# Performance work log

Measured on AMD Instinct MI355X. Metric: run time of the kernel, lower is better.

The kernel has to match this reference:

```python
import jax, jax.numpy as jnp
import numpy as np

N, G, NPG, K = 65536, 64, 1024, 32
NB, BD, IN_CH, GNN_DIM, L = 64, 4, 256, 256, 2
NBP = (BD - 1) * BD // 2 * NB  # 384
E = 524288


def setup_inputs():
    key = jax.random.key(0)
    ks = jax.random.split(key, 10)
    s = 0.05
    return {
        "x": jax.random.normal(ks[0], (N, IN_CH), jnp.float32),
        "eigvec": jax.random.normal(ks[1], (N, K), jnp.float32) / np.float32(np.sqrt(NPG)),
        "eigval": jax.random.uniform(ks[2], (G, K), jnp.float32, 0.0, 2.0),
        "taus": jnp.ones((NB,), jnp.float32),
        "enc_w": jax.random.normal(ks[3], (IN_CH, GNN_DIM), jnp.float32) * s,
        "enc_b": jnp.zeros((GNN_DIM,), jnp.float32),
        "self_w": jax.random.normal(ks[4], (L, GNN_DIM, GNN_DIM), jnp.float32) * s,
        "self_b": jnp.zeros((L, GNN_DIM), jnp.float32),
        "nb_w": jax.random.normal(ks[5], (L, GNN_DIM, GNN_DIM), jnp.float32) * s,
        "nb_b": jnp.zeros((L, GNN_DIM), jnp.float32),
        "dec_w": jax.random.normal(ks[6], (GNN_DIM, NBP), jnp.float32) * s,
        "dec_b": jnp.zeros((NBP,), jnp.float32),
        "lin_w": jax.random.normal(ks[7], (IN_CH, IN_CH), jnp.float32) * s,
        "lin_b": jnp.zeros((IN_CH,), jnp.float32),
        "edge_index": jax.random.randint(ks[8], (2, E), 0, N, jnp.int32),
    }


def _householder(p):
    # p: [M, BD*(BD-1)//2] -> Q: [M, BD, BD], product of BD-1 Householder reflectors
    M = p.shape[0]
    Q = jnp.broadcast_to(jnp.eye(BD, dtype=p.dtype), (M, BD, BD))
    idx = 0
    for j in range(BD - 1):  # small fixed loop over bundle_dim-1 reflectors
        n = BD - 1 - j
        v = jnp.zeros((M, BD), p.dtype).at[:, j].set(1.0)
        v = v.at[:, j + 1:].set(p[:, idx:idx + n])
        idx += n
        nrm = jnp.sum(v * v, axis=1)[:, None, None]
        Qv = jnp.einsum('mij,mj->mi', Q, v)
        Q = Q - 2.0 * Qv[:, :, None] * v[:, None, :] / nrm
    return Q


def reference(x, eigvec, eigval, taus, enc_w, enc_b, self_w, self_b,
              nb_w, nb_b, dec_w, dec_b, lin_w, lin_b, edge_index):
    gelu = lambda t: jax.nn.gelu(t, approximate=False)
    src, dst = edge_index[0], edge_index[1]
    vf = x.reshape(N, NB, BD, -1)                      # [N, NB, BD, 1]
    # SumGNN structural encoder: h = gelu(enc(x)); residual GNN layers; dec
    h = gelu(x @ enc_w + enc_b)
    for k in range(L):
        agg = jax.ops.segment_sum(h[src], dst, num_segments=N)  # sum aggregation
        hk = (h @ self_w[k] + self_b[k]) + (agg @ nb_w[k] + nb_b[k])
        h = gelu(hk) + h
    node_rep = h @ dec_w + dec_b                       # [N, NBP]
    Q = _householder(node_rep.reshape(N * NB, NBP // NB)).reshape(N, NB, BD, BD)
    vf = jnp.einsum('abcd,abde->abce', Q, vf)          # bundle transform
    h = vf.reshape(G, NPG, IN_CH)                      # to_dense_batch (equal-size graphs)
    ev = eigvec.reshape(G, NPG, K)
    hs = jnp.einsum('gnv,gnd->gvd', ev, h)             # project onto eigenbasis
    fact = jnp.exp(-eigval[:, :, None] * taus[None, None, :])   # [G, K, NB]
    hs = (hs.reshape(G, K, NB, BD, -1) * fact[..., None, None]).reshape(G, K, IN_CH)
    h = jnp.einsum('gnv,gvd->gnd', ev, hs).reshape(N, IN_CH)     # reproject
    h = h @ lin_w + lin_b
    vf = jnp.einsum('abdc,abde->abce', Q, h.reshape(N, NB, BD, -1))  # Q^T
    return vf.reshape(N, IN_CH)
```

## Files before the change

### kernel.cpp

```cpp
#include <hip/hip_runtime.h>
#include <math.h>

#define NN      65536
#define GG      64
#define NPG     1024
#define KEIG    32
#define NBUN    64
#define BDIM    4
#define CH      256
#define NBP     384
#define NEDGE   524288

using f16x8 = __attribute__((ext_vector_type(8))) _Float16;
using f16x4 = __attribute__((ext_vector_type(4))) _Float16;
using f32x4 = __attribute__((ext_vector_type(4))) float;

__device__ __forceinline__ float gelu_f(float x) {
    return 0.5f * x * (1.0f + erff(x * 0.70710678118654752440f));
}

template<int NOUT, int KTOT, bool DUAL, bool ACT, bool RESA, bool WF, bool W16>
__global__ __launch_bounds__(NOUT, 2) void mgemm_k(
    const _Float16* __restrict__ A1, const _Float16* __restrict__ A2,
    const _Float16* __restrict__ Bp, const float* __restrict__ bias,
    float* __restrict__ Cf, _Float16* __restrict__ C16)
{
    constexpr int NT   = KTOT / 32;
    constexpr int ROWB = KTOT * 2;
    constexpr int CPR  = KTOT / 8;
    constexpr int CTS  = NOUT + 8;
    constexpr int AH   = 64 * KTOT;
    constexpr int CTH  = 64 * CTS;
    constexpr int LDSH = (W16 && CTH > AH) ? CTH : AH;
    __shared__ _Float16 Alds[LDSH];

    const int tid  = threadIdx.x;
    const int lane = tid & 63;
    const int wave = tid >> 6;
    const int m0   = blockIdx.x * 64;

    const int r16 = lane & 15;
    const int kc  = lane >> 4;

    const _Float16* bpp = Bp + ((size_t)wave * NT * 2048) + lane * 8;

    f16x8 pa0, pa1, pa2, pa3, pb0, pb1, pb2, pb3;
    f16x8 pc0, pc1, pc2, pc3, pd0, pd1, pd2, pd3;

#define LDB(P0, P1, P2, P3, T)                                                 \
    {                                                                          \
        const _Float16* bq_ = bpp + (size_t)(T) * 2048;                        \
        P0 = *(const f16x8*)(bq_);                                             \
        P1 = *(const f16x8*)(bq_ + 512);                                       \
        P2 = *(const f16x8*)(bq_ + 1024);                                      \
        P3 = *(const f16x8*)(bq_ + 1536);                                      \
    }

    LDB(pa0, pa1, pa2, pa3, 0)
    LDB(pb0, pb1, pb2, pb3, 1)
    LDB(pc0, pc1, pc2, pc3, 2)
    LDB(pd0, pd1, pd2, pd3, 3)

    constexpr int TOTC = 64 * CPR;
    constexpr int NSTG = TOTC / NOUT;
    {
        f16x8 stg[NSTG ? NSTG : 1];
#pragma unroll
        for (int j = 0; j < NSTG; j++) {
            const int idx = tid + j * NOUT;
            const int r = idx / CPR, c = idx - r * CPR;
            const _Float16* src = (DUAL && c >= CPR / 2)
                ? A2 + (size_t)(m0 + r) * 256 + (c - CPR / 2) * 8
                : A1 + (size_t)(m0 + r) * 256 + c * 8;
            stg[j] = *(const f16x8*)src;
        }
#pragma unroll
        for (int j = 0; j < NSTG; j++) {
            const int idx = tid + j * NOUT;
            const int r = idx / CPR, c = idx - r * CPR;
            *(f16x8*)((char*)Alds + ((r * ROWB + c * 16) ^ ((r & 7) << 4))) = stg[j];
        }
        if (TOTC % NOUT) {
            const int idx = tid + NSTG * NOUT;
            if (idx < TOTC) {
                const int r = idx / CPR, c = idx - r * CPR;
                const _Float16* src = (DUAL && c >= CPR / 2)
                    ? A2 + (size_t)(m0 + r) * 256 + (c - CPR / 2) * 8
                    : A1 + (size_t)(m0 + r) * 256 + c * 8;
                f16x8 v = *(const f16x8*)src;
                *(f16x8*)((char*)Alds + ((r * ROWB + c * 16) ^ ((r & 7) << 4))) = v;
            }
        }
    }
    __syncthreads();

    f32x4 acc[4][4];
#pragma unroll
    for (int i = 0; i < 4; i++)
#pragma unroll
        for (int j = 0; j < 4; j++) acc[i][j] = 0.f;

#define MSTEP(OFF, P0, P1, P2, P3)                                             \
    {                                                                          \
        const char* ap_ = (const char*)Alds + (OFF);                           \
        f16x8 a0_ = *(const f16x8*)(ap_);                                      \
        f16x8 a1_ = *(const f16x8*)(ap_ + 16 * ROWB);                          \
        f16x8 a2_ = *(const f16x8*)(ap_ + 32 * ROWB);                          \
        f16x8 a3_ = *(const f16x8*)(ap_ + 48 * ROWB);                          \
        acc[0][0] = __builtin_amdgcn_mfma_f32_16x16x32_f16(a0_, P0, acc[0][0], 0, 0, 0); \
        acc[0][1] = __builtin_amdgcn_mfma_f32_16x16x32_f16(a0_, P1, acc[0][1], 0, 0, 0); \
        acc[0][2] = __builtin_amdgcn_mfma_f32_16x16x32_f16(a0_, P2, acc[0][2], 0, 0, 0); \
        acc[0][3] = __builtin_amdgcn_mfma_f32_16x16x32_f16(a0_, P3, acc[0][3], 0, 0, 0); \
        acc[1][0] = __builtin_amdgcn_mfma_f32_16x16x32_f16(a1_, P0, acc[1][0], 0, 0, 0); \
        acc[1][1] = __builtin_amdgcn_mfma_f32_16x16x32_f16(a1_, P1, acc[1][1], 0, 0, 0); \
        acc[1][2] = __builtin_amdgcn_mfma_f32_16x16x32_f16(a1_, P2, acc[1][2], 0, 0, 0); \
        acc[1][3] = __builtin_amdgcn_mfma_f32_16x16x32_f16(a1_, P3, acc[1][3], 0, 0, 0); \
        acc[2][0] = __builtin_amdgcn_mfma_f32_16x16x32_f16(a2_, P0, acc[2][0], 0, 0, 0); \
        acc[2][1] = __builtin_amdgcn_mfma_f32_16x16x32_f16(a2_, P1, acc[2][1], 0, 0, 0); \
        acc[2][2] = __builtin_amdgcn_mfma_f32_16x16x32_f16(a2_, P2, acc[2][2], 0, 0, 0); \
        acc[2][3] = __builtin_amdgcn_mfma_f32_16x16x32_f16(a2_, P3, acc[2][3], 0, 0, 0); \
        acc[3][0] = __builtin_amdgcn_mfma_f32_16x16x32_f16(a3_, P0, acc[3][0], 0, 0, 0); \
        acc[3][1] = __builtin_amdgcn_mfma_f32_16x16x32_f16(a3_, P1, acc[3][1], 0, 0, 0); \
        acc[3][2] = __builtin_amdgcn_mfma_f32_16x16x32_f16(a3_, P2, acc[3][2], 0, 0, 0); \
        acc[3][3] = __builtin_amdgcn_mfma_f32_16x16x32_f16(a3_, P3, acc[3][3], 0, 0, 0); \
    }

    int au = r16 * ROWB + kc * 16;
    const int swz = (r16 & 7) << 4;
#pragma unroll
    for (int t = 0; t < NT; t += 4) {
        MSTEP((au      ) ^ swz, pa0, pa1, pa2, pa3)
        if (t + 4 < NT) LDB(pa0, pa1, pa2, pa3, t + 4)
        MSTEP((au +  64) ^ swz, pb0, pb1, pb2, pb3)
        if (t + 5 < NT) LDB(pb0, pb1, pb2, pb3, t + 5)
        MSTEP((au + 128) ^ swz, pc0, pc1, pc2, pc3)
        if (t + 6 < NT) LDB(pc0, pc1, pc2, pc3, t + 6)
        MSTEP((au + 192) ^ swz, pd0, pd1, pd2, pd3)
        if (t + 7 < NT) LDB(pd0, pd1, pd2, pd3, t + 7)
        au += 256;
    }
#undef LDB
#undef MSTEP

    const int rbase = (lane >> 4) * 4;
    const int ncol  = lane & 15;
    if constexpr (W16) {
        __syncthreads();
#pragma unroll
        for (int nt = 0; nt < 4; nt++) {
            const int n = wave * 64 + nt * 16 + ncol;
            const float bs = bias[n];
#pragma unroll
            for (int mt = 0; mt < 4; mt++) {
#pragma unroll
                for (int i = 0; i < 4; i++) {
                    const int mr = mt * 16 + rbase + i;
                    float v = acc[mt][nt][i] + bs;
                    if (ACT) v = gelu_f(v);
                    if (RESA) v += (float)A1[(size_t)(m0 + mr) * 256 + n];
                    Alds[mr * CTS + n] = (_Float16)v;
                }
            }
        }
        __syncthreads();
        constexpr int CPRN = NOUT / 8;
        constexpr int CPT  = 64 * CPRN / NOUT;
#pragma unroll
        for (int k2 = 0; k2 < CPT; k2++) {
            const int c = tid + k2 * NOUT;
            const int row = c / CPRN, col = c - row * CPRN;
            f16x8 v = *(const f16x8*)&Alds[row * CTS + col * 8];
            *(f16x8*)(C16 + (size_t)(m0 + row) * NOUT + col * 8) = v;
        }
    } else {
#pragma unroll
        for (int nt = 0; nt < 4; nt++) {
            const int n = wave * 64 + nt * 16 + ncol;
            const float bs = bias[n];
#pragma unroll
            for (int mt = 0; mt < 4; mt++) {
#pragma unroll
                for (int i = 0; i < 4; i++) {
                    const int m = m0 + mt * 16 + rbase + i;
                    float v = acc[mt][nt][i] + bs;
                    if (ACT) v = gelu_f(v);
                    if (RESA) v += (float)A1[(size_t)m * 256 + n];
                    if (WF) Cf[(size_t)m * NOUT + n] = v;
                }
            }
        }
    }
}

template<int NOUT, int KTOT, bool DUAL>
__global__ __launch_bounds__(256) void pack_k(
    const float* __restrict__ W1, const float* __restrict__ W2,
    _Float16* __restrict__ Bp)
{
    constexpr int NT = KTOT / 32;
    const int cid = blockIdx.x * 256 + threadIdx.x;
    if (cid >= NOUT * KTOT / 8) return;
    const int l  = cid & 63;
    const int q  = (cid >> 6) & 3;
    const int c2 = cid >> 8;
    const int t  = c2 & (NT - 1);
    const int wn = c2 / NT;
    const int n  = wn * 64 + q * 16 + (l & 15);
    const int k0 = t * 32 + (l >> 4) * 8;
    f16x8 v;
#pragma unroll
    for (int j = 0; j < 8; j++) {
        const int k = k0 + j;
        float w = (DUAL && k >= 256) ? W2[(size_t)(k - 256) * NOUT + n]
                                     : W1[(size_t)k * NOUT + n];
        v[j] = (_Float16)w;
    }
    *(f16x8*)(Bp + (size_t)cid * 8) = v;
}

__global__ void zero_k(float* __restrict__ p, size_t n)
{
    size_t i = (size_t)blockIdx.x * blockDim.x + threadIdx.x;
    float4* p4 = (float4*)p;
    size_t n4 = n >> 2;
    for (size_t j = i; j < n4; j += (size_t)gridDim.x * blockDim.x)
        p4[j] = make_float4(0.f, 0.f, 0.f, 0.f);
}

__global__ __launch_bounds__(256) void cvt16_k(
    const float* __restrict__ in, _Float16* __restrict__ out)
{
    size_t i = (size_t)blockIdx.x * 256 + threadIdx.x;
    float4 v = ((const float4*)in)[i];
    f16x4 o = { (_Float16)v.x, (_Float16)v.y, (_Float16)v.z, (_Float16)v.w };
    ((f16x4*)out)[i] = o;
}

__global__ void bcomb_k(const float* __restrict__ a, const float* __restrict__ b,
                        float* __restrict__ o)
{
    int i = blockIdx.x * 256 + threadIdx.x;
    if (i < 512) o[i] = a[i] + b[i];
}

__global__ __launch_bounds__(256) void hist_k(const int* __restrict__ ei, int* __restrict__ deg)
{
    int e = blockIdx.x * 256 + threadIdx.x;
    if (e < NEDGE) atomicAdd(&deg[ei[NEDGE + e]], 1);
}

__global__ __launch_bounds__(1024) void scan_k(
    const int* __restrict__ deg, int* __restrict__ off, int* __restrict__ cursor)
{
    __shared__ int sh[1024];
    const int tid = threadIdx.x;
    const int base = tid * 64;
    int s = 0;
#pragma unroll 8
    for (int i = 0; i < 64; i++) s += deg[base + i];
    const int mysum = s;
    sh[tid] = s;
    __syncthreads();
    for (int ofs = 1; ofs < 1024; ofs <<= 1) {
        int v = (tid >= ofs) ? sh[tid - ofs] : 0;
        __syncthreads();
        sh[tid] += v;
        __syncthreads();
    }
    int running = sh[tid] - mysum;
    for (int i = 0; i < 64; i++) {
        off[base + i] = running;
        cursor[base + i] = running;
        running += deg[base + i];
    }
    if (tid == 1023) off[NN] = running;
}

__global__ __launch_bounds__(256) void fill_k(
    const int* __restrict__ ei, int* __restrict__ cursor, int* __restrict__ csr)
{
    int e = blockIdx.x * 256 + threadIdx.x;
    if (e < NEDGE) {
        int d = ei[NEDGE + e];
        int pos = atomicAdd(&cursor[d], 1);
        csr[pos] = ei[e];
    }
}

__global__ __launch_bounds__(256) void gather16_k(
    const _Float16* __restrict__ h, const int* __restrict__ off,
    const int* __restrict__ csr, _Float16* __restrict__ agg)
{
    const int lane = threadIdx.x & 63;
    const int n = blockIdx.x * 4 + (threadIdx.x >> 6);
    const int s0 = off[n], s1 = off[n + 1];
    float a0 = 0.f, a1 = 0.f, a2 = 0.f, a3 = 0.f;
    int j = s0;
    for (; j + 3 < s1; j += 4) {
        const int i0 = csr[j], i1 = csr[j + 1], i2 = csr[j + 2], i3 = csr[j + 3];
        f16x4 v0 = ((const f16x4*)(h + (size_t)i0 * CH))[lane];
        f16x4 v1 = ((const f16x4*)(h + (size_t)i1 * CH))[lane];
        f16x4 v2 = ((const f16x4*)(h + (size_t)i2 * CH))[lane];
        f16x4 v3 = ((const f16x4*)(h + (size_t)i3 * CH))[lane];
        a0 += (float)v0[0] + (float)v1[0] + (float)v2[0] + (float)v3[0];
        a1 += (float)v0[1] + (float)v1[1] + (float)v2[1] + (float)v3[1];
        a2 += (float)v0[2] + (float)v1[2] + (float)v2[2] + (float)v3[2];
        a3 += (float)v0[3] + (float)v1[3] + (float)v2[3] + (float)v3[3];
    }
    for (; j < s1; j++) {
        f16x4 va = ((const f16x4*)(h + (size_t)csr[j] * CH))[lane];
        a0 += (float)va[0]; a1 += (float)va[1]; a2 += (float)va[2]; a3 += (float)va[3];
    }
    f16x4 o = { (_Float16)a0, (_Float16)a1, (_Float16)a2, (_Float16)a3 };
    ((f16x4*)(agg + (size_t)n * CH))[lane] = o;
}

__device__ __forceinline__ void make_Q(const _Float16* __restrict__ p, float Q[4][4])
{
#pragma unroll
    for (int i = 0; i < 4; i++)
#pragma unroll
        for (int j = 0; j < 4; j++) Q[i][j] = (i == j) ? 1.f : 0.f;
    int idx = 0;
#pragma unroll
    for (int j = 0; j < 3; j++) {
        float v[4] = {0.f, 0.f, 0.f, 0.f};
        v[j] = 1.f;
#pragma unroll
        for (int t = 0; t < 4; t++)
            if (t > j) v[t] = (float)p[idx + t - (j + 1)];
        idx += 3 - j;
        float nrm = v[0]*v[0] + v[1]*v[1] + v[2]*v[2] + v[3]*v[3];
        float s = 2.f / nrm;
#pragma unroll
        for (int i = 0; i < 4; i++) {
            float qv = Q[i][0]*v[0] + Q[i][1]*v[1] + Q[i][2]*v[2] + Q[i][3]*v[3];
            float t0 = s * qv;
#pragma unroll
            for (int c = 0; c < 4; c++) Q[i][c] -= t0 * v[c];
        }
    }
}

template<bool TRANS>
__global__ __launch_bounds__(256) void bundle_k(
    const float* __restrict__ vin, const _Float16* __restrict__ nr,
    float* __restrict__ out)
{
    __shared__ _Float16 pb[4 * NBP];
    const int n0 = blockIdx.x * 4;
    for (int i = threadIdx.x; i < 4 * NBP; i += 256)
        pb[i] = nr[(size_t)n0 * NBP + i];
    __syncthreads();
    const int ln = threadIdx.x >> 6;
    const int b  = threadIdx.x & 63;
    const int n  = n0 + ln;
    float Q[4][4];
    make_Q(&pb[ln * NBP + b * 6], Q);
    float4 xv = ((const float4*)(vin + (size_t)n * CH))[b];
    float in0 = xv.x, in1 = xv.y, in2 = xv.z, in3 = xv.w;
    float4 o;
    if constexpr (!TRANS) {
        o.x = Q[0][0]*in0 + Q[0][1]*in1 + Q[0][2]*in2 + Q[0][3]*in3;
        o.y = Q[1][0]*in0 + Q[1][1]*in1 + Q[1][2]*in2 + Q[1][3]*in3;
        o.z = Q[2][0]*in0 + Q[2][1]*in1 + Q[2][2]*in2 + Q[2][3]*in3;
        o.w = Q[3][0]*in0 + Q[3][1]*in1 + Q[3][2]*in2 + Q[3][3]*in3;
    } else {
        o.x = Q[0][0]*in0 + Q[1][0]*in1 + Q[2][0]*in2 + Q[3][0]*in3;
        o.y = Q[0][1]*in0 + Q[1][1]*in1 + Q[2][1]*in2 + Q[3][1]*in3;
        o.z = Q[0][2]*in0 + Q[1][2]*in1 + Q[2][2]*in2 + Q[3][2]*in3;
        o.w = Q[0][3]*in0 + Q[1][3]*in1 + Q[2][3]*in2 + Q[3][3]*in3;
    }
    ((float4*)(out + (size_t)n * CH))[b] = o;
}

__global__ __launch_bounds__(256) void spec_proj_k(
    const float* __restrict__ v, const float* __restrict__ eigvec, float* __restrict__ hs)
{
    const int g = blockIdx.x;
    const int nbase = g * NPG + blockIdx.y * 128;
    __shared__ float evs[16][32];
    float acc[32];
#pragma unroll
    for (int k = 0; k < 32; k++) acc[k] = 0.f;
    for (int nt = 0; nt < 128; nt += 16) {
        __syncthreads();
        for (int i = threadIdx.x; i < 512; i += 256) {
            int nn = i >> 5, kk = i & 31;
            evs[nn][kk] = eigvec[(size_t)(nbase + nt + nn) * KEIG + kk];
        }
        __syncthreads();
#pragma unroll 4
        for (int nn = 0; nn < 16; nn++) {
            float hv = v[(size_t)(nbase + nt + nn) * CH + threadIdx.x];
#pragma unroll
            for (int k = 0; k < 32; k++) acc[k] += evs[nn][k] * hv;
        }
    }
    float* o = hs + (size_t)g * KEIG * CH + threadIdx.x;
#pragma unroll
    for (int k = 0; k < 32; k++) atomicAdd(o + k * CH, acc[k]);
}

__global__ __launch_bounds__(256) void spec_reproj16_k(
    const float* __restrict__ eigvec, const float* __restrict__ hs,
    const float* __restrict__ eigval, const float* __restrict__ taus,
    _Float16* __restrict__ out16)
{
    const int g = blockIdx.x >> 4;
    const int nbase = g * NPG + (blockIdx.x & 15) * 64;
    const float tau = taus[threadIdx.x >> 2];
    float hsr[32];
    const float* hg = hs + (size_t)g * KEIG * CH + threadIdx.x;
#pragma unroll
    for (int k = 0; k < 32; k++)
        hsr[k] = hg[k * CH] * expf(-eigval[g * KEIG + k] * tau);
    __shared__ float evs[64][32];
    for (int i = threadIdx.x; i < 2048; i += 256) {
        int nn = i >> 5, kk = i & 31;
        evs[nn][kk] = eigvec[(size_t)(nbase + nn) * KEIG + kk];
    }
    __syncthreads();
    for (int nn = 0; nn < 64; nn++) {
        float a = 0.f;
#pragma unroll
        for (int k = 0; k < 32; k++) a += evs[nn][k] * hsr[k];
        out16[(size_t)(nbase + nn) * CH + threadIdx.x] = (_Float16)a;
    }
}

extern "C" void kernel_launch(void* const* d_in, const int* in_sizes, int n_in,
                              void* d_out, int out_size, void* d_ws, size_t ws_size,
                              hipStream_t stream)
{
    const float* x      = (const float*)d_in[0];
    const float* eigvec = (const float*)d_in[1];
    const float* eigval = (const float*)d_in[2];
    const float* taus   = (const float*)d_in[3];
    const float* enc_w  = (const float*)d_in[4];
    const float* enc_b  = (const float*)d_in[5];
    const float* self_w = (const float*)d_in[6];
    const float* self_b = (const float*)d_in[7];
    const float* nb_w   = (const float*)d_in[8];
    const float* nb_b   = (const float*)d_in[9];
    const float* dec_w  = (const float*)d_in[10];
    const float* dec_b  = (const float*)d_in[11];
    const float* lin_w  = (const float*)d_in[12];
    const float* lin_b  = (const float*)d_in[13];
    const int*   ei     = (const int*)d_in[14];
    (void)in_sizes; (void)n_in; (void)out_size; (void)ws_size;

    float* ws = (float*)d_ws;
    _Float16* x16 = (_Float16*)(ws);
    _Float16* h0  = (_Float16*)(ws + 8388608);
    _Float16* h1  = (_Float16*)(ws + 16777216);
    _Float16* agg = (_Float16*)(ws + 25165824);
    int* ibase  = (int*)(ws + 33554432);
    int* deg    = ibase;
    int* off    = ibase + 65536;
    int* cursor = ibase + 131073;
    int* csr    = ibase + 196609;
    _Float16* nr16 = (_Float16*)(ws + 25165824);
    float* wb = ws + 37748752;
    _Float16* enc16 = (_Float16*)(wb);
    _Float16* l1w   = (_Float16*)(wb + 32768);
    _Float16* l2w   = (_Float16*)(wb + 98304);
    _Float16* dec16 = (_Float16*)(wb + 163840);
    _Float16* lin16 = (_Float16*)(wb + 212992);
    float* lbias = wb + 245760;
    _Float16* h2 = (_Float16*)(ws + 37995024);
    float* vf1 = ws;
    float* hs  = ws + 16777216;
    float* h3  = vf1;

    dim3 blk(256);

    cvt16_k<<<16384, blk, 0, stream>>>(x, x16);
    pack_k<256, 256, false><<<32, blk, 0, stream>>>(enc_w, nullptr, enc16);
    pack_k<256, 512, true ><<<64, blk, 0, stream>>>(self_w,         nb_w,         l1w);
    pack_k<256, 512, true ><<<64, blk, 0, stream>>>(self_w + 65536, nb_w + 65536, l2w);
    pack_k<384, 256, false><<<48, blk, 0, stream>>>(dec_w, nullptr, dec16);
    pack_k<256, 256, false><<<32, blk, 0, stream>>>(lin_w, nullptr, lin16);
    bcomb_k<<<2, blk, 0, stream>>>(self_b, nb_b, lbias);
    zero_k<<<64, blk, 0, stream>>>((float*)deg, (size_t)NN);
    hist_k<<<NEDGE / 256, blk, 0, stream>>>(ei, deg);
    scan_k<<<1, 1024, 0, stream>>>(deg, off, cursor);
    fill_k<<<NEDGE / 256, blk, 0, stream>>>(ei, cursor, csr);

    mgemm_k<256, 256, false, true, false, false, true><<<dim3(1024), blk, 0, stream>>>(
        x16, nullptr, enc16, enc_b, nullptr, h0);

    gather16_k<<<NN / 4, blk, 0, stream>>>(h0, off, csr, agg);
    mgemm_k<256, 512, true, true, true, false, true><<<dim3(1024), blk, 0, stream>>>(
        h0, agg, l1w, lbias, nullptr, h1);

    gather16_k<<<NN / 4, blk, 0, stream>>>(h1, off, csr, agg);
    mgemm_k<256, 512, true, true, true, false, true><<<dim3(1024), blk, 0, stream>>>(
        h1, agg, l2w, lbias + 256, nullptr, h0);

    mgemm_k<384, 256, false, false, false, false, true><<<dim3(1024), dim3(384), 0, stream>>>(
        h0, nullptr, dec16, dec_b, nullptr, nr16);

    bundle_k<false><<<NN / 4, blk, 0, stream>>>(x, nr16, vf1);

    zero_k<<<512, blk, 0, stream>>>(hs, (size_t)GG * KEIG * CH);
    spec_proj_k<<<dim3(GG, 8), blk, 0, stream>>>(vf1, eigvec, hs);
    spec_reproj16_k<<<GG * 16, blk, 0, stream>>>(eigvec, hs, eigval, taus, h2);

    mgemm_k<256, 256, false, false, false, true, false><<<dim3(1024), blk, 0, stream>>>(
        h2, nullptr, lin16, lin_b, h3, nullptr);

    bundle_k<true><<<NN / 4, blk, 0, stream>>>(h3, nr16, (float*)d_out);
}
```

Measured before the change: 694.2 us.

## Stage dual-input GEMM A operand in halves to cut LDS and raise occupancy

The fused GEMM kernel now stages only a 64x256 A tile in LDS at a time. For the dual-input (K=512) variant it loads A1, computes, then syncs and restages A2, which halves LDS usage. Launch bounds are raised to 4 or 3 blocks per SM to match. The fp16 epilogue also loads the residual with vector reads and adds it in half precision after the LDS transpose, where the fp32 path did scalar reads. The tradeoffs are an extra barrier and load stall mid-kernel, possible register pressure from the higher occupancy target, and reduced precision on the residual add.

```diff
diff --git a/kernel.cpp b/kernel.cpp
--- a/kernel.cpp
+++ b/kernel.cpp
@@ -20,16 +20,19 @@
 }
 
 template<int NOUT, int KTOT, bool DUAL, bool ACT, bool RESA, bool WF, bool W16>
-__global__ __launch_bounds__(NOUT, 2) void mgemm_k(
+__global__ __launch_bounds__(NOUT, (NOUT == 256) ? 4 : 3) void mgemm_k(
     const _Float16* __restrict__ A1, const _Float16* __restrict__ A2,
     const _Float16* __restrict__ Bp, const float* __restrict__ bias,
     float* __restrict__ Cf, _Float16* __restrict__ C16)
 {
     constexpr int NT   = KTOT / 32;
-    constexpr int ROWB = KTOT * 2;
-    constexpr int CPR  = KTOT / 8;
+    constexpr int HALVES = KTOT / 256;
+    constexpr int ROWB = 512;
+    constexpr int CPR  = 32;
+    constexpr int TOTC = 64 * CPR;
+    constexpr int NSTG = TOTC / NOUT;
     constexpr int CTS  = NOUT + 8;
-    constexpr int AH   = 64 * KTOT;
+    constexpr int AH   = 64 * 256;
     constexpr int CTH  = 64 * CTS;
     constexpr int LDSH = (W16 && CTH > AH) ? CTH : AH;
     __shared__ _Float16 Alds[LDSH];
@@ -56,42 +59,37 @@
         P3 = *(const f16x8*)(bq_ + 1536);                                      \
     }
 
+#define STAGE(BASE)                                                            \
+    {                                                                          \
+        f16x8 stg[NSTG];                                                       \
+        _Pragma("unroll")                                                      \
+        for (int j = 0; j < NSTG; j++) {                                       \
+            const int idx = tid + j * NOUT;                                    \
+            const int r = idx >> 5, c = idx & 31;                              \
+            stg[j] = *(const f16x8*)((BASE) + (size_t)(m0 + r) * 256 + c * 8); \
+        }                                                                      \
+        _Pragma("unroll")                                                      \
+        for (int j = 0; j < NSTG; j++) {                                       \
+            const int idx = tid + j * NOUT;                                    \
+            const int r = idx >> 5, c = idx & 31;                              \
+            *(f16x8*)((char*)Alds + ((r * ROWB + c * 16) ^ ((r & 7) << 4))) = stg[j]; \
+        }                                                                      \
+        if (TOTC % NOUT) {                                                     \
+            const int idx = tid + NSTG * NOUT;                                 \
+            if (idx < TOTC) {                                                  \
+                const int r = idx >> 5, c = idx & 31;                          \
+                f16x8 v = *(const f16x8*)((BASE) + (size_t)(m0 + r) * 256 + c * 8); \
+                *(f16x8*)((char*)Alds + ((r * ROWB + c * 16) ^ ((r & 7) << 4))) = v; \
+            }                                                                  \
+        }                                                                      \
+    }
+
     LDB(pa0, pa1, pa2, pa3, 0)
     LDB(pb0, pb1, pb2, pb3, 1)
     LDB(pc0, pc1, pc2, pc3, 2)
     LDB(pd0, pd1, pd2, pd3, 3)
 
-    constexpr int TOTC = 64 * CPR;
-    constexpr int NSTG = TOTC / NOUT;
-    {
-        f16x8 stg[NSTG ? NSTG : 1];
-#pragma unroll
-        for (int j = 0; j < NSTG; j++) {
-            const int idx = tid + j * NOUT;
-            const int r = idx / CPR, c = idx - r * CPR;
-            const _Float16* src = (DUAL && c >= CPR / 2)
-                ? A2 + (size_t)(m0 + r) * 256 + (c - CPR / 2) * 8
-                : A1 + (size_t)(m0 + r) * 256 + c * 8;
-            stg[j] = *(const f16x8*)src;
-        }
-#pragma unroll
-        for (int j = 0; j < NSTG; j++) {
-            const int idx = tid + j * NOUT;
-            const int r = idx / CPR, c = idx - r * CPR;
-            *(f16x8*)((char*)Alds + ((r * ROWB + c * 16) ^ ((r & 7) << 4))) = stg[j];
-        }
-        if (TOTC % NOUT) {
-            const int idx = tid + NSTG * NOUT;
-            if (idx < TOTC) {
-                const int r = idx / CPR, c = idx - r * CPR;
-                const _Float16* src = (DUAL && c >= CPR / 2)
-                    ? A2 + (size_t)(m0 + r) * 256 + (c - CPR / 2) * 8
-                    : A1 + (size_t)(m0 + r) * 256 + c * 8;
-                f16x8 v = *(const f16x8*)src;
-                *(f16x8*)((char*)Alds + ((r * ROWB + c * 16) ^ ((r & 7) << 4))) = v;
-            }
-        }
-    }
+    STAGE(A1)
     __syncthreads();
 
     f32x4 acc[4][4];
@@ -125,27 +123,48 @@
         acc[3][3] = __builtin_amdgcn_mfma_f32_16x16x32_f16(a3_, P3, acc[3][3], 0, 0, 0); \
     }
 
-    int au = r16 * ROWB + kc * 16;
     const int swz = (r16 & 7) << 4;
 #pragma unroll
-    for (int t = 0; t < NT; t += 4) {
-        MSTEP((au      ) ^ swz, pa0, pa1, pa2, pa3)
-        if (t + 4 < NT) LDB(pa0, pa1, pa2, pa3, t + 4)
-        MSTEP((au +  64) ^ swz, pb0, pb1, pb2, pb3)
-        if (t + 5 < NT) LDB(pb0, pb1, pb2, pb3, t + 5)
-        MSTEP((au + 128) ^ swz, pc0, pc1, pc2, pc3)
-        if (t + 6 < NT) LDB(pc0, pc1, pc2, pc3, t + 6)
-        MSTEP((au + 192) ^ swz, pd0, pd1, pd2, pd3)
-        if (t + 7 < NT) LDB(pd0, pd1, pd2, pd3, t + 7)
-        au += 256;
+    for (int h = 0; h < HALVES; ++h) {
+        if (h > 0) {
+            __syncthreads();
+            STAGE(A2)
+            __syncthreads();
+        }
+        int au = r16 * ROWB + kc * 16;
+#pragma unroll
+        for (int tt = 0; tt < 8; tt += 4) {
+            const int t = h * 8 + tt;
+            MSTEP((au      ) ^ swz, pa0, pa1, pa2, pa3)
+            if (t + 4 < NT) LDB(pa0, pa1, pa2, pa3, t + 4)
+            MSTEP((au +  64) ^ swz, pb0, pb1, pb2, pb3)
+            if (t + 5 < NT) LDB(pb0, pb1, pb2, pb3, t + 5)
+            MSTEP((au + 128) ^ swz, pc0, pc1, pc2, pc3)
+            if (t + 6 < NT) LDB(pc0, pc1, pc2, pc3, t + 6)
+            MSTEP((au + 192) ^ swz, pd0, pd1, pd2, pd3)
+            if (t + 7 < NT) LDB(pd0, pd1, pd2, pd3, t + 7)
+            au += 256;
+        }
     }
 #undef LDB
 #undef MSTEP
+#undef STAGE
 
     const int rbase = (lane >> 4) * 4;
     const int ncol  = lane & 15;
     if constexpr (W16) {
         __syncthreads();
+        constexpr int CPRN = NOUT / 8;
+        constexpr int CPT  = 64 * CPRN / NOUT;
+        f16x8 res[CPT];
+        if constexpr (RESA) {
+#pragma unroll
+            for (int k2 = 0; k2 < CPT; k2++) {
+                const int c = tid + k2 * NOUT;
+                const int row = c / CPRN, col = c - row * CPRN;
+                res[k2] = *(const f16x8*)(A1 + (size_t)(m0 + row) * 256 + col * 8);
+            }
+        }
 #pragma unroll
         for (int nt = 0; nt < 4; nt++) {
             const int n = wave * 64 + nt * 16 + ncol;
@@ -157,19 +176,17 @@
                     const int mr = mt * 16 + rbase + i;
                     float v = acc[mt][nt][i] + bs;
                     if (ACT) v = gelu_f(v);
-                    if (RESA) v += (float)A1[(size_t)(m0 + mr) * 256 + n];
                     Alds[mr * CTS + n] = (_Float16)v;
                 }
             }
         }
         __syncthreads();
-        constexpr int CPRN = NOUT / 8;
-        constexpr int CPT  = 64 * CPRN / NOUT;
 #pragma unroll
         for (int k2 = 0; k2 < CPT; k2++) {
             const int c = tid + k2 * NOUT;
             const int row = c / CPRN, col = c - row * CPRN;
             f16x8 v = *(const f16x8*)&Alds[row * CTS + col * 8];
+            if constexpr (RESA) v = v + res[k2];
             *(f16x8*)(C16 + (size_t)(m0 + row) * NOUT + col * 8) = v;
         }
     } else {
```

New measurement: 702.5 us. Within noise of the previous version (+1.2%).
